# Kernel optimization log

Measured on AMD Instinct MI355X. Metric: run time of the kernel, lower is better.

The kernel has to match this reference:

```python
import jax, jax.numpy as jnp
import numpy as np

CHANNELS = [4096, 4096, 4096, 4096]
SPARSITY = 0.9  # fraction of weight entries zeroed (sten.random_mask_sparsify frac)
BATCH = 4096


def _sparse_weight(key, out_f, in_f, frac):
    kw, km = jax.random.split(key)
    w = jax.random.normal(kw, (out_f, in_f), dtype=jnp.float32)
    keep = jax.random.uniform(km, (out_f, in_f)) >= frac  # keep ~(1-frac) entries
    return jnp.where(keep, w, 0.0)


def setup_inputs() -> dict:
    key = jax.random.key(0)
    ks = jax.random.split(key, 7)
    x = jax.random.normal(ks[0], (BATCH, CHANNELS[0]), dtype=jnp.float32)
    W1 = _sparse_weight(ks[1], CHANNELS[1], CHANNELS[0], SPARSITY)
    b1 = jax.random.uniform(ks[2], (CHANNELS[1],), dtype=jnp.float32)
    W2 = _sparse_weight(ks[3], CHANNELS[2], CHANNELS[1], SPARSITY)
    b2 = jax.random.uniform(ks[4], (CHANNELS[2],), dtype=jnp.float32)
    W3 = _sparse_weight(ks[5], CHANNELS[3], CHANNELS[2], SPARSITY)
    b3 = jax.random.uniform(ks[6], (CHANNELS[3],), dtype=jnp.float32)
    return {"x": x, "W1": W1, "b1": b1, "W2": W2, "b2": b2, "W3": W3, "b3": b3}


def reference(x, W1, b1, W2, b2, W3, b3):
    # Sequential: Linear -> ReLU -> Linear -> ReLU -> Linear
    # F.linear(x, W, b) == x @ W.T + b; weights already carry the sparsity mask.
    h = x @ W1.T + b1
    h = jax.nn.relu(h)
    h = h @ W2.T + b2
    h = jax.nn.relu(h)
    return h @ W3.T + b3
```

## Files before the change

kernel.cpp:

```cpp
#include <hip/hip_runtime.h>
#include <cstdint>


#define MATN 4096

typedef _Float16 half8 __attribute__((ext_vector_type(8)));
typedef float f32x4 __attribute__((ext_vector_type(4)));

__device__ __forceinline__ void glds16(const void* g, const void* l) {
    __builtin_amdgcn_global_load_lds(
        (const __attribute__((address_space(1))) char*)(uintptr_t)g,
        (__attribute__((address_space(3))) char*)(uintptr_t)l,
        16, 0, 0);
}

__global__ __launch_bounds__(256)
void cvt_f16(const float* __restrict__ in, _Float16* __restrict__ out) {
    size_t i = ((size_t)blockIdx.x * 256 + threadIdx.x) * 8;
    const float4* p = (const float4*)(in + i);
    float4 a = p[0];
    float4 b = p[1];
    half8 o;
    o[0] = (_Float16)a.x; o[1] = (_Float16)a.y;
    o[2] = (_Float16)a.z; o[3] = (_Float16)a.w;
    o[4] = (_Float16)b.x; o[5] = (_Float16)b.y;
    o[6] = (_Float16)b.z; o[7] = (_Float16)b.w;
    *(half8*)(out + i) = o;
}

template <bool RELU, typename OutT>
__global__ __launch_bounds__(256, 4)
void gemm_bt(const _Float16* __restrict__ A, const _Float16* __restrict__ B,
             const float* __restrict__ bias, OutT* __restrict__ C) {
    __shared__ _Float16 sA[128 * 32];
    __shared__ _Float16 sB[128 * 32];

    const int tid  = threadIdx.x;
    const int lane = tid & 63;
    const int w    = tid >> 6;
    const int wm   = w >> 1;
    const int wn   = w & 1;
    const int l16  = lane & 15;
    const int kq   = lane >> 4;

    const int tileM = blockIdx.y * 128;
    const int tileN = blockIdx.x * 128;

    f32x4 acc[4][4] = {};

    const int r0 = tid >> 2;
    const int gc = ((tid & 3) ^ ((tid >> 3) & 3)) * 8;

    const _Float16* Ap0 = A + (size_t)(tileM + r0) * MATN + gc;
    const _Float16* Ap1 = Ap0 + (size_t)64 * MATN;
    const _Float16* Bp0 = B + (size_t)(tileN + r0) * MATN + gc;
    const _Float16* Bp1 = Bp0 + (size_t)64 * MATN;

    char* sAb0 = (char*)sA + w * 1024;
    char* sAb1 = sAb0 + 4096;
    char* sBb0 = (char*)sB + w * 1024;
    char* sBb1 = sBb0 + 4096;

    const int slot = kq ^ ((l16 >> 1) & 3);
    const _Float16* rA = sA + (wm * 64 + l16) * 32 + slot * 8;
    const _Float16* rB = sB + (wn * 64 + l16) * 32 + slot * 8;

    for (int k0 = 0; k0 < MATN; k0 += 32) {
        glds16(Ap0, sAb0);
        glds16(Ap1, sAb1);
        glds16(Bp0, sBb0);
        glds16(Bp1, sBb1);
        Ap0 += 32; Ap1 += 32; Bp0 += 32; Bp1 += 32;
        __syncthreads();

        half8 af[4], bf[4];
#pragma unroll
        for (int mi = 0; mi < 4; ++mi)
            af[mi] = *(const half8*)(rA + mi * 512);
#pragma unroll
        for (int ni = 0; ni < 4; ++ni)
            bf[ni] = *(const half8*)(rB + ni * 512);

#pragma unroll
        for (int mi = 0; mi < 4; ++mi)
#pragma unroll
            for (int ni = 0; ni < 4; ++ni)
                acc[mi][ni] = __builtin_amdgcn_mfma_f32_16x16x32_f16(
                    af[mi], bf[ni], acc[mi][ni], 0, 0, 0);
        __syncthreads();
    }

#pragma unroll
    for (int ni = 0; ni < 4; ++ni) {
        const int gn = tileN + wn * 64 + ni * 16 + l16;
        const float bv = bias[gn];
#pragma unroll
        for (int mi = 0; mi < 4; ++mi) {
            const int gm = tileM + wm * 64 + mi * 16 + kq * 4;
#pragma unroll
            for (int r = 0; r < 4; ++r) {
                float v = acc[mi][ni][r] + bv;
                if (RELU) v = v > 0.f ? v : 0.f;
                C[(size_t)(gm + r) * MATN + gn] = (OutT)v;
            }
        }
    }
}

extern "C" void kernel_launch(void* const* d_in, const int* in_sizes, int n_in,
                              void* d_out, int out_size, void* d_ws, size_t ws_size,
                              hipStream_t stream) {
    const float* x  = (const float*)d_in[0];
    const float* W1 = (const float*)d_in[1];
    const float* b1 = (const float*)d_in[2];
    const float* W2 = (const float*)d_in[3];
    const float* b2 = (const float*)d_in[4];
    const float* W3 = (const float*)d_in[5];
    const float* b3 = (const float*)d_in[6];
    float* out = (float*)d_out;

    const size_t MAT = (size_t)MATN * MATN;
    _Float16* xb = (_Float16*)d_ws;
    _Float16* wb = (_Float16*)((char*)d_ws + MAT * 2);
    _Float16* h1 = (_Float16*)((char*)d_ws + MAT * 4);
    _Float16* h2 = xb;

    const int cblocks = (int)(MAT / (8 * 256));
    dim3 ggrid(MATN / 128, MATN / 128);

    cvt_f16<<<cblocks, 256, 0, stream>>>(x, xb);
    cvt_f16<<<cblocks, 256, 0, stream>>>(W1, wb);
    gemm_bt<true, _Float16><<<ggrid, 256, 0, stream>>>(xb, wb, b1, h1);

    cvt_f16<<<cblocks, 256, 0, stream>>>(W2, wb);
    gemm_bt<true, _Float16><<<ggrid, 256, 0, stream>>>(h1, wb, b2, h2);

    cvt_f16<<<cblocks, 256, 0, stream>>>(W3, wb);
    gemm_bt<false, float><<<ggrid, 256, 0, stream>>>(h2, wb, b3, out);
}
```

Before: 691.1 us.

## Fuse fp32-to-fp16 conversion into GEMM tile loads, drop separate convert kernels

Removes the four standalone fp32-to-fp16 conversion kernels and templates the GEMM on input element type. fp32 operands are loaded directly into LDS with an 8-way XOR swizzle and converted to fp16 in registers before the MFMA. This saves the extra global read/write passes and kernel launches for conversion. In exchange it doubles global and LDS traffic for fp32 operands inside every tile, since each weight element is re-read across all M-tiles. It also adds conversion ALU work to the inner loop and lowers the occupancy hint from 4 to 3.

```diff
diff --git a/kernel.cpp b/kernel.cpp
--- a/kernel.cpp
+++ b/kernel.cpp
@@ -7,33 +7,23 @@
 typedef _Float16 half8 __attribute__((ext_vector_type(8)));
 typedef float f32x4 __attribute__((ext_vector_type(4)));
 
-__device__ __forceinline__ void glds16(const void* g, const void* l) {
+__device__ __forceinline__ void glds16(const void* g, void* l) {
     __builtin_amdgcn_global_load_lds(
         (const __attribute__((address_space(1))) char*)(uintptr_t)g,
         (__attribute__((address_space(3))) char*)(uintptr_t)l,
         16, 0, 0);
 }
 
-__global__ __launch_bounds__(256)
-void cvt_f16(const float* __restrict__ in, _Float16* __restrict__ out) {
-    size_t i = ((size_t)blockIdx.x * 256 + threadIdx.x) * 8;
-    const float4* p = (const float4*)(in + i);
-    float4 a = p[0];
-    float4 b = p[1];
-    half8 o;
-    o[0] = (_Float16)a.x; o[1] = (_Float16)a.y;
-    o[2] = (_Float16)a.z; o[3] = (_Float16)a.w;
-    o[4] = (_Float16)b.x; o[5] = (_Float16)b.y;
-    o[6] = (_Float16)b.z; o[7] = (_Float16)b.w;
-    *(half8*)(out + i) = o;
-}
+template <bool RELU, typename AT, typename BT, typename OutT>
+__global__ __launch_bounds__(256, 3)
+void gemm_bt(const AT* __restrict__ A, const BT* __restrict__ B,
+             const float* __restrict__ bias, OutT* __restrict__ C) {
+    constexpr int ASZ = (int)sizeof(AT);
+    constexpr int BSZ = (int)sizeof(BT);
+    constexpr int AR  = ASZ == 2 ? 2 : 4;
+    constexpr int BR  = BSZ == 2 ? 2 : 4;
 
-template <bool RELU, typename OutT>
-__global__ __launch_bounds__(256, 4)
-void gemm_bt(const _Float16* __restrict__ A, const _Float16* __restrict__ B,
-             const float* __restrict__ bias, OutT* __restrict__ C) {
-    __shared__ _Float16 sA[128 * 32];
-    __shared__ _Float16 sB[128 * 32];
+    __shared__ char smem[(ASZ + BSZ) * 4096];
 
     const int tid  = threadIdx.x;
     const int lane = tid & 63;
@@ -48,38 +38,91 @@
 
     f32x4 acc[4][4] = {};
 
-    const int r0 = tid >> 2;
-    const int gc = ((tid & 3) ^ ((tid >> 3) & 3)) * 8;
+    const AT* Ap[AR];
+    if constexpr (ASZ == 2) {
+        const int r = tid >> 2;
+        const int g = (tid & 3) ^ ((tid >> 3) & 3);
+        const AT* p = A + (size_t)(tileM + r) * MATN + g * 8;
+#pragma unroll
+        for (int c = 0; c < AR; ++c) Ap[c] = p + (size_t)(64 * c) * MATN;
+    } else {
+        const int r = tid >> 3;
+        const int g = (tid & 7) ^ ((tid >> 3) & 7);
+        const AT* p = A + (size_t)(tileM + r) * MATN + g * 4;
+#pragma unroll
+        for (int c = 0; c < AR; ++c) Ap[c] = p + (size_t)(32 * c) * MATN;
+    }
+    const BT* Bp[BR];
+    if constexpr (BSZ == 2) {
+        const int r = tid >> 2;
+        const int g = (tid & 3) ^ ((tid >> 3) & 3);
+        const BT* p = B + (size_t)(tileN + r) * MATN + g * 8;
+#pragma unroll
+        for (int c = 0; c < BR; ++c) Bp[c] = p + (size_t)(64 * c) * MATN;
+    } else {
+        const int r = tid >> 3;
+        const int g = (tid & 7) ^ ((tid >> 3) & 7);
+        const BT* p = B + (size_t)(tileN + r) * MATN + g * 4;
+#pragma unroll
+        for (int c = 0; c < BR; ++c) Bp[c] = p + (size_t)(32 * c) * MATN;
+    }
 
-    const _Float16* Ap0 = A + (size_t)(tileM + r0) * MATN + gc;
-    const _Float16* Ap1 = Ap0 + (size_t)64 * MATN;
-    const _Float16* Bp0 = B + (size_t)(tileN + r0) * MATN + gc;
-    const _Float16* Bp1 = Bp0 + (size_t)64 * MATN;
+    char* sAl = smem + w * 1024;
+    char* sBl = smem + ASZ * 4096 + w * 1024;
 
-    char* sAb0 = (char*)sA + w * 1024;
-    char* sAb1 = sAb0 + 4096;
-    char* sBb0 = (char*)sB + w * 1024;
-    char* sBb1 = sBb0 + 4096;
-
-    const int slot = kq ^ ((l16 >> 1) & 3);
-    const _Float16* rA = sA + (wm * 64 + l16) * 32 + slot * 8;
-    const _Float16* rB = sB + (wn * 64 + l16) * 32 + slot * 8;
-
-    for (int k0 = 0; k0 < MATN; k0 += 32) {
-        glds16(Ap0, sAb0);
-        glds16(Ap1, sAb1);
-        glds16(Bp0, sBb0);
-        glds16(Bp1, sBb1);
-        Ap0 += 32; Ap1 += 32; Bp0 += 32; Bp1 += 32;
+    for (int k0 = 0; k0 < MATN / 32; ++k0) {
+#pragma unroll
+        for (int c = 0; c < AR; ++c) { glds16(Ap[c], sAl + c * 4096); Ap[c] += 32; }
+#pragma unroll
+        for (int c = 0; c < BR; ++c) { glds16(Bp[c], sBl + c * 4096); Bp[c] += 32; }
         __syncthreads();
 
         half8 af[4], bf[4];
+        if constexpr (ASZ == 2) {
+            const _Float16* rA = (const _Float16*)smem
+                + (wm * 64 + l16) * 32 + (kq ^ ((l16 >> 1) & 3)) * 8;
 #pragma unroll
-        for (int mi = 0; mi < 4; ++mi)
-            af[mi] = *(const half8*)(rA + mi * 512);
+            for (int mi = 0; mi < 4; ++mi)
+                af[mi] = *(const half8*)(rA + mi * 512);
+        } else {
+            const float* rA = (const float*)smem + (wm * 64 + l16) * 32;
+            const int s0 = (2 * kq) ^ (l16 & 7);
+            const int s1 = (2 * kq + 1) ^ (l16 & 7);
 #pragma unroll
-        for (int ni = 0; ni < 4; ++ni)
-            bf[ni] = *(const half8*)(rB + ni * 512);
+            for (int mi = 0; mi < 4; ++mi) {
+                float4 lo = *(const float4*)(rA + mi * 512 + s0 * 4);
+                float4 hi = *(const float4*)(rA + mi * 512 + s1 * 4);
+                half8 f;
+                f[0] = (_Float16)lo.x; f[1] = (_Float16)lo.y;
+                f[2] = (_Float16)lo.z; f[3] = (_Float16)lo.w;
+                f[4] = (_Float16)hi.x; f[5] = (_Float16)hi.y;
+                f[6] = (_Float16)hi.z; f[7] = (_Float16)hi.w;
+                af[mi] = f;
+            }
+        }
+        if constexpr (BSZ == 2) {
+            const _Float16* rB = (const _Float16*)(smem + ASZ * 4096)
+                + (wn * 64 + l16) * 32 + (kq ^ ((l16 >> 1) & 3)) * 8;
+#pragma unroll
+            for (int ni = 0; ni < 4; ++ni)
+                bf[ni] = *(const half8*)(rB + ni * 512);
+        } else {
+            const float* rB = (const float*)(smem + ASZ * 4096)
+                + (wn * 64 + l16) * 32;
+            const int s0 = (2 * kq) ^ (l16 & 7);
+            const int s1 = (2 * kq + 1) ^ (l16 & 7);
+#pragma unroll
+            for (int ni = 0; ni < 4; ++ni) {
+                float4 lo = *(const float4*)(rB + ni * 512 + s0 * 4);
+                float4 hi = *(const float4*)(rB + ni * 512 + s1 * 4);
+                half8 f;
+                f[0] = (_Float16)lo.x; f[1] = (_Float16)lo.y;
+                f[2] = (_Float16)lo.z; f[3] = (_Float16)lo.w;
+                f[4] = (_Float16)hi.x; f[5] = (_Float16)hi.y;
+                f[6] = (_Float16)hi.z; f[7] = (_Float16)hi.w;
+                bf[ni] = f;
+            }
+        }
 
 #pragma unroll
         for (int mi = 0; mi < 4; ++mi)
@@ -120,21 +163,12 @@
     float* out = (float*)d_out;
 
     const size_t MAT = (size_t)MATN * MATN;
-    _Float16* xb = (_Float16*)d_ws;
-    _Float16* wb = (_Float16*)((char*)d_ws + MAT * 2);
-    _Float16* h1 = (_Float16*)((char*)d_ws + MAT * 4);
-    _Float16* h2 = xb;
+    _Float16* h1 = (_Float16*)d_ws;
+    _Float16* h2 = (_Float16*)((char*)d_ws + MAT * 2);
 
-    const int cblocks = (int)(MAT / (8 * 256));
     dim3 ggrid(MATN / 128, MATN / 128);
 
-    cvt_f16<<<cblocks, 256, 0, stream>>>(x, xb);
-    cvt_f16<<<cblocks, 256, 0, stream>>>(W1, wb);
-    gemm_bt<true, _Float16><<<ggrid, 256, 0, stream>>>(xb, wb, b1, h1);
-
-    cvt_f16<<<cblocks, 256, 0, stream>>>(W2, wb);
-    gemm_bt<true, _Float16><<<ggrid, 256, 0, stream>>>(h1, wb, b2, h2);
-
-    cvt_f16<<<cblocks, 256, 0, stream>>>(W3, wb);
-    gemm_bt<false, float><<<ggrid, 256, 0, stream>>>(h2, wb, b3, out);
+    gemm_bt<true,  float,    float, _Float16><<<ggrid, 256, 0, stream>>>(x,  W1, b1, h1);
+    gemm_bt<true,  _Float16, float, _Float16><<<ggrid, 256, 0, stream>>>(h1, W2, b2, h2);
+    gemm_bt<false, _Float16, float, float   ><<<ggrid, 256, 0, stream>>>(h2, W3, b3, out);
 }
```

After: 858.3 us. 1.24x slower.
